# Optimization experiments

Hardware: AMD Instinct MI355X
Metric: run time of the kernel (lower is better)

Reference implementation:

```python
import jax, jax.numpy as jnp
from jax import lax
import numpy as np

V, E, H, L, C = 50257, 128, 128, 2, 32
B, T = 64, 2048


def setup_inputs() -> dict:
    key = jax.random.key(0)
    ks = jax.random.split(key, 12)
    s_e = 1.0 / np.sqrt(H)  # torch GRU init scale
    inp = {
        'x': jax.random.randint(ks[0], (B, T), 0, V),
        'emb': jax.random.normal(ks[1], (V, E), jnp.float32),
        'w_ih0': jax.random.uniform(ks[2], (3 * H, E), jnp.float32, -s_e, s_e),
        'w_hh0': jax.random.uniform(ks[3], (3 * H, H), jnp.float32, -s_e, s_e),
        'b_ih0': jax.random.uniform(ks[4], (3 * H,), jnp.float32, -s_e, s_e),
        'b_hh0': jax.random.uniform(ks[5], (3 * H,), jnp.float32, -s_e, s_e),
        'w_ih1': jax.random.uniform(ks[6], (3 * H, H), jnp.float32, -s_e, s_e),
        'w_hh1': jax.random.uniform(ks[7], (3 * H, H), jnp.float32, -s_e, s_e),
        'b_ih1': jax.random.uniform(ks[8], (3 * H,), jnp.float32, -s_e, s_e),
        'b_hh1': jax.random.uniform(ks[9], (3 * H,), jnp.float32, -s_e, s_e),
        'fc_w': jax.random.uniform(ks[10], (C, H), jnp.float32, -s_e, s_e),
        'fc_b': jax.random.uniform(ks[11], (C,), jnp.float32, -s_e, s_e),
    }
    return inp


def _gru_layer(x_tbe, w_ih, w_hh, b_ih, b_hh):
    # x_tbe: [T, B, Din]; torch GRU gate order: r, z, n
    gi = jnp.einsum('tbd,gd->tbg', x_tbe, w_ih) + b_ih  # [T, B, 3H] precomputed input gates
    h0 = jnp.zeros((x_tbe.shape[1], w_hh.shape[0] // 3), x_tbe.dtype)

    def step(h, gi_t):
        gh = h @ w_hh.T + b_hh
        ir, iz, inn = jnp.split(gi_t, 3, axis=-1)
        hr, hz, hn = jnp.split(gh, 3, axis=-1)
        r = jax.nn.sigmoid(ir + hr)
        z = jax.nn.sigmoid(iz + hz)
        n = jnp.tanh(inn + r * hn)
        h_new = (1.0 - z) * n + z * h
        return h_new, h_new

    _, ys = lax.scan(step, h0, gi)
    return ys  # [T, B, H]


def reference(x, emb, w_ih0, w_hh0, b_ih0, b_hh0, w_ih1, w_hh1, b_ih1, b_hh1, fc_w, fc_b):
    e = emb[x]                      # [B, T, E] embedding lookup
    h = jnp.swapaxes(e, 0, 1)       # [T, B, E] (time-major for scan)
    h = _gru_layer(h, w_ih0, w_hh0, b_ih0, b_hh0)
    h = _gru_layer(h, w_ih1, w_hh1, b_ih1, b_hh1)
    y = jnp.swapaxes(h, 0, 1)       # [B, T, H]
    out = jax.nn.relu(y @ fc_w.T + fc_b)  # [B, T, C]
    return out.reshape(-1, out.shape[-1])  # [B*T, C]
```

## Files before the change

kernel.cpp:

```cpp
#include <hip/hip_runtime.h>
#include <math.h>

#define B_ 64
#define T_ 2048
#define E_ 128
#define H_ 128
#define G3_ 384
#define C_ 32
#define M_ (T_ * B_)
#define CH_ 16
#define NCH_ (T_ / CH_)

typedef _Float16 f16x2 __attribute__((ext_vector_type(2)));

__device__ __forceinline__ f16x2 as_h2(unsigned int u) {
    union { unsigned int u; f16x2 h; } c; c.u = u; return c.h;
}

#if __has_builtin(__builtin_amdgcn_fdot2)
__device__ __forceinline__ float fdot2_acc(f16x2 a, f16x2 b, float c) {
    return __builtin_amdgcn_fdot2(a, b, c, false);
}
#else
__device__ __forceinline__ float fdot2_acc(f16x2 a, f16x2 b, float c) {
    return fmaf((float)a.y, (float)b.y, fmaf((float)a.x, (float)b.x, c));
}
#endif

__device__ __forceinline__ void wait_ge(int* f, int need) {
    while (__hip_atomic_load(f, __ATOMIC_ACQUIRE, __HIP_MEMORY_SCOPE_AGENT) < need)
        __builtin_amdgcn_s_sleep(8);
}

#define DOT96(HSRC, S0, S1, S2)                                                \
  {                                                                            \
    float a00 = 0.f, a01 = 0.f, a10 = 0.f, a11 = 0.f, a20 = 0.f, a21 = 0.f;    \
    _Pragma("unroll")                                                          \
    for (int i = 0; i < 8; i++) {                                              \
      uint4 u = (HSRC)[i];                                                     \
      f16x2 ux = as_h2(u.x), uy = as_h2(u.y), uz = as_h2(u.z), uw = as_h2(u.w);\
      a00 = fdot2_acc(wr[0][4*i+0], ux, a00);                                  \
      a10 = fdot2_acc(wr[1][4*i+0], ux, a10);                                  \
      a20 = fdot2_acc(wr[2][4*i+0], ux, a20);                                  \
      a01 = fdot2_acc(wr[0][4*i+1], uy, a01);                                  \
      a11 = fdot2_acc(wr[1][4*i+1], uy, a11);                                  \
      a21 = fdot2_acc(wr[2][4*i+1], uy, a21);                                  \
      a00 = fdot2_acc(wr[0][4*i+2], uz, a00);                                  \
      a10 = fdot2_acc(wr[1][4*i+2], uz, a10);                                  \
      a20 = fdot2_acc(wr[2][4*i+2], uz, a20);                                  \
      a01 = fdot2_acc(wr[0][4*i+3], uw, a01);                                  \
      a11 = fdot2_acc(wr[1][4*i+3], uw, a11);                                  \
      a21 = fdot2_acc(wr[2][4*i+3], uw, a21);                                  \
    }                                                                          \
    S0 = a00 + a01; S1 = a10 + a11; S2 = a20 + a21;                            \
  }

#define GSTEPX(CUR, NXT, IR, IZ, INN, TT, TP)                                  \
  {                                                                            \
    const uint4* hsrc = (const uint4*)((const char*)hb[CUR] + kh * 128);       \
    float s0, s1, s2;                                                          \
    DOT96(hsrc, s0, s1, s2);                                                   \
    const float hr = s0 + __shfl_xor(s0, 1) + bg0;                             \
    const float hz = s1 + __shfl_xor(s1, 1) + bg1;                             \
    const float hn = s2 + __shfl_xor(s2, 1) + bg2;                             \
    const float rr = 1.f / (1.f + __expf(-((IR) + hr)));                       \
    const float zz = 1.f / (1.f + __expf(-((IZ) + hz)));                       \
    const float na = (INN) + rr * hn;                                          \
    const float nn = 1.f - 2.f / (__expf(2.f * na) + 1.f);                     \
    h_own = (1.f - zz) * nn + zz * h_own;                                      \
    if (kh == 0) hb[NXT][g] = (_Float16)h_own;                                 \
    else         y_g[(size_t)(TT) * (B_ * H_)] = h_own;                        \
    {                                                                          \
      const int tp = ((TP) < T_) ? (TP) : (TT);                                \
      const float* gp = gi_g + (size_t)tp * (B_ * G3_);                        \
      IR = gp[0]; IZ = gp[128]; INN = gp[256];                                 \
    }                                                                          \
    asm volatile("s_waitcnt lgkmcnt(0)" ::: "memory");                         \
    __builtin_amdgcn_s_barrier();                                              \
    __builtin_amdgcn_sched_barrier(0);                                         \
  }

__global__ __launch_bounds__(256, 1) void gru_pipe(
    const float* __restrict__ emb,
    const int*   __restrict__ xidx,
    const float* __restrict__ w_ih0,
    const float* __restrict__ b_ih0,
    float* __restrict__ gi,
    const float* __restrict__ w_hh0,
    const float* __restrict__ b_hh0,
    const float* __restrict__ w_ih1,
    const float* __restrict__ b_ih1,
    const float* __restrict__ w_hh1,
    const float* __restrict__ b_hh1,
    float* __restrict__ ybuf,
    int* __restrict__ flags)
{
    const int tid = threadIdx.x;
    const int w   = tid >> 6;
    const int l   = tid & 63;
    const int g   = w * 32 + (l >> 1);
    const int kh  = l & 1;
    const int role = blockIdx.x >> 6;
    const int b    = blockIdx.x & 63;
    int* q0 = flags + b;
    int* p0 = flags + 64 + b;
    int* p1 = flags + 128 + b;

    __shared__ __align__(16) _Float16 hb[2][128];
    __shared__ __align__(16) f16x2 srow[16][64];

    if (role == 0 || role == 2) {
        const float* wsrc = (role == 0) ? w_ih0 : w_ih1;
        const float* bsrc = (role == 0) ? b_ih0 : b_ih1;
        f16x2 wr[3][32];
#pragma unroll
        for (int G = 0; G < 3; G++) {
            const float2* w2 = (const float2*)(wsrc + (size_t)(g + 128 * G) * 128 + kh * 64);
#pragma unroll
            for (int i = 0; i < 32; i++) {
                float2 v = w2[i];
                wr[G][i] = (f16x2){(_Float16)v.x, (_Float16)v.y};
            }
        }
        const float c0 = bsrc[g], c1 = bsrc[g + 128], c2 = bsrc[g + 256];

        for (int c = 0; c < NCH_; c++) {
            if (role == 2) {
                if (tid == 0) wait_ge(p0, (c + 1) * CH_);
            }
            __syncthreads();
            for (int j = tid; j < 16 * 64; j += 256) {
                const int s = j >> 6, p = j & 63;
                const float* src;
                if (role == 0) {
                    const long row = (long)xidx[b * T_ + c * CH_ + s];
                    src = emb + row * 128;
                } else {
                    src = ybuf + ((size_t)(c * CH_ + s) * B_ + b) * H_;
                }
                const float2 v = ((const float2*)src)[p];
                srow[s][p] = (f16x2){(_Float16)v.x, (_Float16)v.y};
            }
            __syncthreads();
            for (int s = 0; s < 16; s++) {
                const uint4* hsrc = (const uint4*)srow[s] + kh * 8;
                float s0, s1, s2;
                DOT96(hsrc, s0, s1, s2);
                const float r0v = s0 + __shfl_xor(s0, 1);
                const float r1v = s1 + __shfl_xor(s1, 1);
                const float r2v = s2 + __shfl_xor(s2, 1);
                if (kh == 0) {
                    float* go = gi + ((size_t)(c * CH_ + s) * B_ + b) * G3_ + g;
                    go[0]   = r0v + c0;
                    go[128] = r1v + c1;
                    go[256] = r2v + c2;
                }
            }
            asm volatile("s_waitcnt vmcnt(0)" ::: "memory");
            __syncthreads();
            if (tid == 0) {
                int* rel = (role == 0) ? q0 : p1;
                __hip_atomic_store(rel, c + 1, __ATOMIC_RELEASE, __HIP_MEMORY_SCOPE_AGENT);
            }
        }
        return;
    }

    const float* wsrc = (role == 3) ? w_hh1 : w_hh0;
    const float* bsrc = (role == 3) ? b_hh1 : b_hh0;
    int* wf = (role == 3) ? p1 : q0;

    f16x2 wr[3][32];
#pragma unroll
    for (int G = 0; G < 3; G++) {
        const float2* w2 = (const float2*)(wsrc + (size_t)(g + 128 * G) * 128 + kh * 64);
#pragma unroll
        for (int i = 0; i < 32; i++) {
            float2 v = w2[i];
            wr[G][i] = (f16x2){(_Float16)v.x, (_Float16)v.y};
        }
    }
    const float bg0 = bsrc[g];
    const float bg1 = bsrc[g + 128];
    const float bg2 = bsrc[g + 256];

    if (tid < 128) hb[0][tid] = (_Float16)0.f;
    float h_own = 0.f;

    const float* gi_g = gi + (size_t)b * G3_ + g;
    float* y_g = ybuf + (size_t)b * H_ + g;

    if (tid == 0) wait_ge(wf, 2);
    __syncthreads();

    float irA = gi_g[0], izA = gi_g[128], innA = gi_g[256];
    const float* pp1 = gi_g + (size_t)(B_ * G3_);
    float irB = pp1[0], izB = pp1[128], innB = pp1[256];

    __syncthreads();

    for (int c = 0; c < NCH_; c++) {
        const int need = (c + 2 < NCH_) ? (c + 2) : NCH_;
        if (tid == 0) wait_ge(wf, need);
        __syncthreads();
        const int t0 = c * CH_;
        for (int i = 0; i < CH_ / 2; i++) {
            const int t = t0 + 2 * i;
            GSTEPX(0, 1, irA, izA, innA, t,     t + 2)
            GSTEPX(1, 0, irB, izB, innB, t + 1, t + 3)
        }
        if (role == 1) {
            asm volatile("s_waitcnt vmcnt(0)" ::: "memory");
            __syncthreads();
            if (tid == 0)
                __hip_atomic_store(p0, (c + 1) * CH_, __ATOMIC_RELEASE, __HIP_MEMORY_SCOPE_AGENT);
        }
    }
}

__global__ __launch_bounds__(256, 2) void fc_relu(
    const float* __restrict__ y,
    const float* __restrict__ fc_w,
    const float* __restrict__ fc_b,
    float* __restrict__ out)
{
    const int tid = threadIdx.x;
    const int c = tid & 31;
    const int slot = tid >> 5;

    float4 wr[32];
    const float4* w4 = (const float4*)(fc_w + c * 128);
#pragma unroll
    for (int i = 0; i < 32; i++) wr[i] = w4[i];
    const float bc = fc_b[c];

    __shared__ __align__(16) float rows[8][128];

    for (int grp = blockIdx.x; grp < M_ / 8; grp += gridDim.x) {
        const int m0 = grp * 8;
        __syncthreads();
        for (int i = tid; i < 8 * 128; i += 256) {
            rows[i >> 7][i & 127] = y[(long)m0 * 128 + i];
        }
        __syncthreads();
        const float4* h4 = (const float4*)rows[slot];
        float a0 = bc, a1 = 0.f, a2 = 0.f, a3 = 0.f;
#pragma unroll
        for (int i = 0; i < 32; i += 4) {
            float4 h0 = h4[i], h1 = h4[i + 1], h2 = h4[i + 2], h3 = h4[i + 3];
            a0 = fmaf(wr[i].w, h0.w, fmaf(wr[i].z, h0.z, fmaf(wr[i].y, h0.y, fmaf(wr[i].x, h0.x, a0))));
            a1 = fmaf(wr[i+1].w, h1.w, fmaf(wr[i+1].z, h1.z, fmaf(wr[i+1].y, h1.y, fmaf(wr[i+1].x, h1.x, a1))));
            a2 = fmaf(wr[i+2].w, h2.w, fmaf(wr[i+2].z, h2.z, fmaf(wr[i+2].y, h2.y, fmaf(wr[i+2].x, h2.x, a2))));
            a3 = fmaf(wr[i+3].w, h3.w, fmaf(wr[i+3].z, h3.z, fmaf(wr[i+3].y, h3.y, fmaf(wr[i+3].x, h3.x, a3))));
        }
        float acc = (a0 + a1) + (a2 + a3);
        acc = fmaxf(acc, 0.f);
        const int m = m0 + slot;
        const int t = m >> 6;
        const int b = m & 63;
        out[((long)b * T_ + t) * C_ + c] = acc;
    }
}

extern "C" void kernel_launch(void* const* d_in, const int* in_sizes, int n_in,
                              void* d_out, int out_size, void* d_ws, size_t ws_size,
                              hipStream_t stream) {
    const int*   x     = (const int*)d_in[0];
    const float* emb   = (const float*)d_in[1];
    const float* w_ih0 = (const float*)d_in[2];
    const float* w_hh0 = (const float*)d_in[3];
    const float* b_ih0 = (const float*)d_in[4];
    const float* b_hh0 = (const float*)d_in[5];
    const float* w_ih1 = (const float*)d_in[6];
    const float* w_hh1 = (const float*)d_in[7];
    const float* b_ih1 = (const float*)d_in[8];
    const float* b_hh1 = (const float*)d_in[9];
    const float* fc_w  = (const float*)d_in[10];
    const float* fc_b  = (const float*)d_in[11];
    float* out = (float*)d_out;

    float* gi   = (float*)d_ws;
    float* ybuf = (float*)((char*)d_ws + (size_t)M_ * G3_ * sizeof(float));

    hipMemsetAsync(d_out, 0, 192 * sizeof(int), stream);

    gru_pipe<<<256, 256, 0, stream>>>(emb, x, w_ih0, b_ih0, gi,
                                      w_hh0, b_hh0, w_ih1, b_ih1, w_hh1, b_hh1,
                                      ybuf, (int*)d_out);
    fc_relu<<<512, 256, 0, stream>>>(ybuf, fc_w, fc_b, out);
}
```

Before: 1.727 ms.

## Split each GRU gate dot product across four lanes with 512-thread blocks

Each hidden unit's recurrent and input-gate dot products are now split across four lanes instead of two, with a two-stage xor-shuffle reduction, and blocks grow from 256 to 512 threads. This halves the serial fdot2 chain per lane on the latency-bound recurrent step and halves the register-resident weights per thread. In exchange there is an extra shuffle round per gate, twice as many waves meeting at each per-step barrier, and duplicated gate math in lanes whose results are discarded.

```diff
diff --git a/kernel.cpp b/kernel.cpp
--- a/kernel.cpp
+++ b/kernel.cpp
@@ -32,11 +32,11 @@
         __builtin_amdgcn_s_sleep(8);
 }
 
-#define DOT96(HSRC, S0, S1, S2)                                                \
+#define DOT48(HSRC, S0, S1, S2)                                                \
   {                                                                            \
     float a00 = 0.f, a01 = 0.f, a10 = 0.f, a11 = 0.f, a20 = 0.f, a21 = 0.f;    \
     _Pragma("unroll")                                                          \
-    for (int i = 0; i < 8; i++) {                                              \
+    for (int i = 0; i < 4; i++) {                                              \
       uint4 u = (HSRC)[i];                                                     \
       f16x2 ux = as_h2(u.x), uy = as_h2(u.y), uz = as_h2(u.z), uw = as_h2(u.w);\
       a00 = fdot2_acc(wr[0][4*i+0], ux, a00);                                  \
@@ -55,21 +55,24 @@
     S0 = a00 + a01; S1 = a10 + a11; S2 = a20 + a21;                            \
   }
 
-#define GSTEPX(CUR, NXT, IR, IZ, INN, TT, TP)                                  \
+#define RED4(S) { S += __shfl_xor(S, 1); S += __shfl_xor(S, 2); }
+
+#define GSTEPQ(CUR, NXT, IR, IZ, INN, TT, TP)                                  \
   {                                                                            \
-    const uint4* hsrc = (const uint4*)((const char*)hb[CUR] + kh * 128);       \
+    const uint4* hsrc = (const uint4*)((const char*)hb[CUR] + kq * 64);        \
     float s0, s1, s2;                                                          \
-    DOT96(hsrc, s0, s1, s2);                                                   \
-    const float hr = s0 + __shfl_xor(s0, 1) + bg0;                             \
-    const float hz = s1 + __shfl_xor(s1, 1) + bg1;                             \
-    const float hn = s2 + __shfl_xor(s2, 1) + bg2;                             \
+    DOT48(hsrc, s0, s1, s2);                                                   \
+    RED4(s0) RED4(s1) RED4(s2)                                                 \
+    const float hr = s0 + bg0;                                                 \
+    const float hz = s1 + bg1;                                                 \
+    const float hn = s2 + bg2;                                                 \
     const float rr = 1.f / (1.f + __expf(-((IR) + hr)));                       \
     const float zz = 1.f / (1.f + __expf(-((IZ) + hz)));                       \
     const float na = (INN) + rr * hn;                                          \
     const float nn = 1.f - 2.f / (__expf(2.f * na) + 1.f);                     \
     h_own = (1.f - zz) * nn + zz * h_own;                                      \
-    if (kh == 0) hb[NXT][g] = (_Float16)h_own;                                 \
-    else         y_g[(size_t)(TT) * (B_ * H_)] = h_own;                        \
+    if (kq == 0) hb[NXT][g] = (_Float16)h_own;                                 \
+    else if (kq == 1) y_g[(size_t)(TT) * (B_ * H_)] = h_own;                   \
     {                                                                          \
       const int tp = ((TP) < T_) ? (TP) : (TT);                                \
       const float* gp = gi_g + (size_t)tp * (B_ * G3_);                        \
@@ -80,7 +83,7 @@
     __builtin_amdgcn_sched_barrier(0);                                         \
   }
 
-__global__ __launch_bounds__(256, 1) void gru_pipe(
+__global__ __launch_bounds__(512, 1) void gru_pipe(
     const float* __restrict__ emb,
     const int*   __restrict__ xidx,
     const float* __restrict__ w_ih0,
@@ -98,8 +101,8 @@
     const int tid = threadIdx.x;
     const int w   = tid >> 6;
     const int l   = tid & 63;
-    const int g   = w * 32 + (l >> 1);
-    const int kh  = l & 1;
+    const int g   = w * 16 + (l >> 2);
+    const int kq  = l & 3;
     const int role = blockIdx.x >> 6;
     const int b    = blockIdx.x & 63;
     int* q0 = flags + b;
@@ -112,12 +115,12 @@
     if (role == 0 || role == 2) {
         const float* wsrc = (role == 0) ? w_ih0 : w_ih1;
         const float* bsrc = (role == 0) ? b_ih0 : b_ih1;
-        f16x2 wr[3][32];
+        f16x2 wr[3][16];
 #pragma unroll
         for (int G = 0; G < 3; G++) {
-            const float2* w2 = (const float2*)(wsrc + (size_t)(g + 128 * G) * 128 + kh * 64);
-#pragma unroll
-            for (int i = 0; i < 32; i++) {
+            const float2* w2 = (const float2*)(wsrc + (size_t)(g + 128 * G) * 128 + kq * 32);
+#pragma unroll
+            for (int i = 0; i < 16; i++) {
                 float2 v = w2[i];
                 wr[G][i] = (f16x2){(_Float16)v.x, (_Float16)v.y};
             }
@@ -129,7 +132,7 @@
                 if (tid == 0) wait_ge(p0, (c + 1) * CH_);
             }
             __syncthreads();
-            for (int j = tid; j < 16 * 64; j += 256) {
+            for (int j = tid; j < 16 * 64; j += 512) {
                 const int s = j >> 6, p = j & 63;
                 const float* src;
                 if (role == 0) {
@@ -143,17 +146,15 @@
             }
             __syncthreads();
             for (int s = 0; s < 16; s++) {
-                const uint4* hsrc = (const uint4*)srow[s] + kh * 8;
+                const uint4* hsrc = (const uint4*)srow[s] + kq * 4;
                 float s0, s1, s2;
-                DOT96(hsrc, s0, s1, s2);
-                const float r0v = s0 + __shfl_xor(s0, 1);
-                const float r1v = s1 + __shfl_xor(s1, 1);
-                const float r2v = s2 + __shfl_xor(s2, 1);
-                if (kh == 0) {
+                DOT48(hsrc, s0, s1, s2);
+                RED4(s0) RED4(s1) RED4(s2)
+                if (kq == 0) {
                     float* go = gi + ((size_t)(c * CH_ + s) * B_ + b) * G3_ + g;
-                    go[0]   = r0v + c0;
-                    go[128] = r1v + c1;
-                    go[256] = r2v + c2;
+                    go[0]   = s0 + c0;
+                    go[128] = s1 + c1;
+                    go[256] = s2 + c2;
                 }
             }
             asm volatile("s_waitcnt vmcnt(0)" ::: "memory");
@@ -170,12 +171,12 @@
     const float* bsrc = (role == 3) ? b_hh1 : b_hh0;
     int* wf = (role == 3) ? p1 : q0;
 
-    f16x2 wr[3][32];
+    f16x2 wr[3][16];
 #pragma unroll
     for (int G = 0; G < 3; G++) {
-        const float2* w2 = (const float2*)(wsrc + (size_t)(g + 128 * G) * 128 + kh * 64);
-#pragma unroll
-        for (int i = 0; i < 32; i++) {
+        const float2* w2 = (const float2*)(wsrc + (size_t)(g + 128 * G) * 128 + kq * 32);
+#pragma unroll
+        for (int i = 0; i < 16; i++) {
             float2 v = w2[i];
             wr[G][i] = (f16x2){(_Float16)v.x, (_Float16)v.y};
         }
@@ -206,8 +207,8 @@
         const int t0 = c * CH_;
         for (int i = 0; i < CH_ / 2; i++) {
             const int t = t0 + 2 * i;
-            GSTEPX(0, 1, irA, izA, innA, t,     t + 2)
-            GSTEPX(1, 0, irB, izB, innB, t + 1, t + 3)
+            GSTEPQ(0, 1, irA, izA, innA, t,     t + 2)
+            GSTEPQ(1, 0, irB, izB, innB, t + 1, t + 3)
         }
         if (role == 1) {
             asm volatile("s_waitcnt vmcnt(0)" ::: "memory");
@@ -284,7 +285,7 @@
 
     hipMemsetAsync(d_out, 0, 192 * sizeof(int), stream);
 
-    gru_pipe<<<256, 256, 0, stream>>>(emb, x, w_ih0, b_ih0, gi,
+    gru_pipe<<<256, 512, 0, stream>>>(emb, x, w_ih0, b_ih0, gi,
                                       w_hh0, b_hh0, w_ih1, b_ih1, w_hh1, b_hh1,
                                       ybuf, (int*)d_out);
     fc_relu<<<512, 256, 0, stream>>>(ybuf, fc_w, fc_b, out);
```

New measurement: 1.926 ms. +11.5%, slower.
